# Kernel tuning notes

Hardware: AMD Instinct MI355X
Metric: run time of the kernel (lower is better)

The kernel has to match this reference:

```python
import jax, jax.numpy as jnp
import numpy as np

B, T, S, H, V, L = 32, 64, 128, 512, 32000, 2  # batch, tgt_len, src_len, d_model, vocab, n_layers


def setup_inputs() -> dict:
    key = jax.random.key(0)
    ks = jax.random.split(key, 14)
    sc = 1.0 / np.sqrt(H)
    tgt = jax.random.randint(ks[0], (B, T), 0, V, dtype=jnp.int32)
    h0 = jax.random.normal(ks[1], (L, B, H), jnp.float32)
    c0 = jax.random.normal(ks[2], (L, B, H), jnp.float32)
    encoder_outputs = jax.random.normal(ks[3], (B, S, H), jnp.float32)
    emb = (jax.random.normal(ks[4], (V, H), jnp.float32) * 0.02).at[0].set(0.0)  # pad_idx=0 row zeroed
    W_ih = jax.random.normal(ks[5], (L, 4 * H, H), jnp.float32) * sc  # gate order i,f,g,o (torch)
    W_hh = jax.random.normal(ks[6], (L, 4 * H, H), jnp.float32) * sc
    b_ih = jax.random.normal(ks[7], (L, 4 * H), jnp.float32) * sc
    b_hh = jax.random.normal(ks[8], (L, 4 * H), jnp.float32) * sc
    Wc = jax.random.normal(ks[9], (H, 2 * H), jnp.float32) * sc
    bc = jax.random.normal(ks[10], (H,), jnp.float32) * sc
    Wo = jax.random.normal(ks[11], (V, H), jnp.float32) * sc
    bo = jax.random.normal(ks[12], (V,), jnp.float32) * sc
    return dict(tgt=tgt, h0=h0, c0=c0, encoder_outputs=encoder_outputs, emb=emb,
                W_ih=W_ih, W_hh=W_hh, b_ih=b_ih, b_hh=b_hh, Wc=Wc, bc=bc, Wo=Wo, bo=bo)


def reference(tgt, h0, c0, encoder_outputs, emb, W_ih, W_hh, b_ih, b_hh, Wc, bc, Wo, bo):
    n_layers = W_ih.shape[0]

    def step(carry, token):
        h, c = carry  # each [L, B, H]
        x = emb[token]  # [B, H]
        hs, cs = [], []
        for l in range(n_layers):  # small fixed structural loop
            gates = x @ W_ih[l].T + b_ih[l] + h[l] @ W_hh[l].T + b_hh[l]  # [B, 4H]
            i_g, f_g, g_g, o_g = jnp.split(gates, 4, axis=-1)
            c_new = jax.nn.sigmoid(f_g) * c[l] + jax.nn.sigmoid(i_g) * jnp.tanh(g_g)
            h_new = jax.nn.sigmoid(o_g) * jnp.tanh(c_new)
            hs.append(h_new)
            cs.append(c_new)
            x = h_new
        out = x  # [B, H] top-layer output
        # Luong (dot) attention over encoder outputs
        scores = jnp.einsum('bh,bsh->bs', out, encoder_outputs)
        attn = jax.nn.softmax(scores, axis=-1)
        context = jnp.einsum('bs,bsh->bh', attn, encoder_outputs)
        out_att = jnp.tanh(jnp.concatenate([out, context], axis=-1) @ Wc.T + bc)
        pred = out_att @ Wo.T + bo  # [B, V]
        return (jnp.stack(hs), jnp.stack(cs)), pred

    (h, c), preds = jax.lax.scan(step, (h0, c0), tgt.T)  # scan over time (T-major)
    return preds.transpose(1, 0, 2), h, c  # [B, T, V], hidden state
```

## Files before the change

### kernel.cpp

```cpp
#include <hip/hip_runtime.h>
#include <hip/hip_bf16.h>

#define Bz 32
#define Tz 64
#define Sz 128
#define Hz 512
#define Vz 32000
#define G4 2048
#define NBLK 256
#define NPH 65

#define A_RLX __ATOMIC_RELAXED
#define SC_AG __HIP_MEMORY_SCOPE_AGENT

using bf16x8 = __attribute__((ext_vector_type(8))) short;
using f32x4  = __attribute__((ext_vector_type(4))) float;

__device__ __forceinline__ unsigned short f2bf(float f){
  unsigned int u = __float_as_uint(f);
  u += 0x7fffu + ((u >> 16) & 1u);
  return (unsigned short)(u >> 16);
}
__device__ __forceinline__ float sigf(float x){ return 1.f/(1.f + expf(-x)); }

__device__ __forceinline__ void stc(float* p, float v){
  __hip_atomic_store(p, v, A_RLX, SC_AG);
}
__device__ __forceinline__ float ldc(const float* p){
  return __hip_atomic_load(p, A_RLX, SC_AG);
}

__device__ __forceinline__ void g_arrive(unsigned* bar, int bid, unsigned e){
  asm volatile("s_waitcnt vmcnt(0)" ::: "memory");
  __syncthreads();
  if (threadIdx.x == 0)
    __hip_atomic_store(&bar[bid], e, A_RLX, SC_AG);
}
__device__ __forceinline__ void g_wait(unsigned* bar, unsigned e){
  if (threadIdx.x < 64){
    const int lane = threadIdx.x;
    for (;;){
      int ok = 1;
      #pragma unroll
      for (int i = 0; i < 4; i++){
        unsigned v = __hip_atomic_load(&bar[lane + i*64], A_RLX, SC_AG);
        ok &= ((int)(v - e) >= 0);
      }
      if (__all(ok)) break;
      __builtin_amdgcn_s_sleep(1);
    }
  }
  __syncthreads();
  __builtin_amdgcn_sched_barrier(0);
}

__device__ __forceinline__ void xreduce(float (&a)[32], int lane){
  #pragma unroll
  for (int j = 0; j < 32; j++) a[j] += __shfl_xor(a[j], 32);
  #pragma unroll
  for (int st = 0; st < 5; st++){
    const int o = 16 >> st;
    bool hi = (lane & o) != 0;
    float tmp[16];
    #pragma unroll
    for (int j = 0; j < o; j++){
      float lo_v = a[j], hi_v = a[j + o];
      float sent = hi ? lo_v : hi_v;
      float recv = __shfl_xor(sent, o);
      tmp[j] = (hi ? hi_v : lo_v) + recv;
    }
    #pragma unroll
    for (int j = 0; j < o; j++) a[j] = tmp[j];
  }
}

__device__ __forceinline__ void stage2c(float* dA, const float* sA,
                                        float* dB, const float* sB, int tid){
  float ra[32], rb[32];
  #pragma unroll
  for (int i = 0; i < 32; i++) ra[i] = ldc(sA + tid + i*512);
  #pragma unroll
  for (int i = 0; i < 32; i++) rb[i] = ldc(sB + tid + i*512);
  #pragma unroll
  for (int i = 0; i < 32; i++){
    int f = tid + i*512;
    dA[(f >> 9)*520 + (f & 511)] = ra[i];
  }
  #pragma unroll
  for (int i = 0; i < 32; i++){
    int f = tid + i*512;
    dB[(f >> 9)*520 + (f & 511)] = rb[i];
  }
}

__global__ __launch_bounds__(256) void init_state_v8(const float* __restrict__ h0,
    float* __restrict__ h0p, float* __restrict__ h1p, unsigned int* __restrict__ bar){
  int i = blockIdx.x*256 + threadIdx.x;
  if (i < 16384) h0p[16384 + i] = h0[i];
  else           h1p[3*16384 + (i - 16384)] = h0[i];
  if (i < 512) bar[i] = 0u;
}

__global__ __launch_bounds__(256) void conv_bf16_kernel(const float* __restrict__ src,
    unsigned short* __restrict__ dst){
  int i = (blockIdx.x*256 + threadIdx.x)*4;
  float4 v = *(const float4*)(src + i);
  ushort4 o;
  o.x = f2bf(v.x); o.y = f2bf(v.y); o.z = f2bf(v.z); o.w = f2bf(v.w);
  *(ushort4*)(dst + i) = o;
}

__global__ __launch_bounds__(256) void pack_l0_v3(const float* __restrict__ W,
    float* __restrict__ out){
  int idx4 = blockIdx.x*256 + threadIdx.x;
  int r = idx4 >> 7, k4 = idx4 & 127;
  int srow = (r & 3)*Hz + (r >> 2);
  ((float4*)out)[idx4] = ((const float4*)W)[srow*128 + k4];
}
__global__ __launch_bounds__(256) void pack_l1_v3(const float* __restrict__ Wi,
    const float* __restrict__ Wh, float* __restrict__ out){
  int idx4 = blockIdx.x*256 + threadIdx.x;
  int r = idx4 >> 8, k4 = idx4 & 255;
  int srow = (r & 3)*Hz + (r >> 2);
  float4 v = (k4 < 128) ? ((const float4*)Wi)[srow*128 + k4]
                        : ((const float4*)Wh)[srow*128 + (k4 - 128)];
  ((float4*)out)[idx4] = v;
}

__global__ __launch_bounds__(256) void x0g_v3(const int* __restrict__ tgt,
    const float* __restrict__ emb, const float* __restrict__ W,
    const float* __restrict__ bi, const float* __restrict__ bh,
    float* __restrict__ out){
  __shared__ float As[32][68], Bs[32][68];
  __shared__ int tok_s[64];
  int tid = threadIdx.x;
  int m0 = blockIdx.y*64, n0 = blockIdx.x*64;
  if (tid < 64){ int tb = m0 + tid; tok_s[tid] = tgt[(tb & 31)*Tz + (tb >> 5)]; }
  __syncthreads();
  int lm = tid >> 2, lk = (tid & 3)*8;
  int ty = tid >> 4, tx = tid & 15;
  float acc[4][4] = {{0.f}};
  for (int kt = 0; kt < 16; kt++){
    float4 a0 = *(const float4*)(emb + (size_t)tok_s[lm]*Hz + kt*32 + lk);
    float4 a1 = *(const float4*)(emb + (size_t)tok_s[lm]*Hz + kt*32 + lk + 4);
    float4 b0 = *(const float4*)(W   + (size_t)(n0+lm)*Hz + kt*32 + lk);
    float4 b1 = *(const float4*)(W   + (size_t)(n0+lm)*Hz + kt*32 + lk + 4);
    __syncthreads();
    As[lk+0][lm]=a0.x; As[lk+1][lm]=a0.y; As[lk+2][lm]=a0.z; As[lk+3][lm]=a0.w;
    As[lk+4][lm]=a1.x; As[lk+5][lm]=a1.y; As[lk+6][lm]=a1.z; As[lk+7][lm]=a1.w;
    Bs[lk+0][lm]=b0.x; Bs[lk+1][lm]=b0.y; Bs[lk+2][lm]=b0.z; Bs[lk+3][lm]=b0.w;
    Bs[lk+4][lm]=b1.x; Bs[lk+5][lm]=b1.y; Bs[lk+6][lm]=b1.z; Bs[lk+7][lm]=b1.w;
    __syncthreads();
    #pragma unroll
    for (int k = 0; k < 32; k++){
      float4 av = *(const float4*)&As[k][ty*4];
      float4 bv = *(const float4*)&Bs[k][tx*4];
      acc[0][0]+=av.x*bv.x; acc[0][1]+=av.x*bv.y; acc[0][2]+=av.x*bv.z; acc[0][3]+=av.x*bv.w;
      acc[1][0]+=av.y*bv.x; acc[1][1]+=av.y*bv.y; acc[1][2]+=av.y*bv.z; acc[1][3]+=av.y*bv.w;
      acc[2][0]+=av.z*bv.x; acc[2][1]+=av.z*bv.y; acc[2][2]+=av.z*bv.z; acc[2][3]+=av.z*bv.w;
      acc[3][0]+=av.w*bv.x; acc[3][1]+=av.w*bv.y; acc[3][2]+=av.w*bv.z; acc[3][3]+=av.w*bv.w;
    }
  }
  #pragma unroll
  for (int j = 0; j < 4; j++){
    int col = n0 + tx*4 + j;
    float bias = bi[col] + bh[col];
    #pragma unroll
    for (int i = 0; i < 4; i++){
      int tb = m0 + ty*4 + i;
      int tt = tb >> 5, bb = tb & 31;
      out[((size_t)tt*2048 + col)*32 + bb] = acc[i][j] + bias;
    }
  }
}

__global__ __launch_bounds__(512, 1) void decoder_persist_v9(
    const float* __restrict__ Wp0, const float* __restrict__ Wp1,
    const float* x0gT,
    const float* __restrict__ bi1, const float* __restrict__ bh1,
    const float* __restrict__ c0in,
    float* __restrict__ h0p,
    float* __restrict__ h1p,
    float* hist,
    float* __restrict__ cbuf,
    unsigned* __restrict__ bar){
  extern __shared__ float sm[];
  float* hstA = sm;
  float* hstB = sm + 16640;
  float* gsA  = sm + 33280;
  float* gsB  = sm + 33792;
  float4* hA4 = (float4*)hstA;
  float4* hB4 = (float4*)hstB;

  const int bid = blockIdx.x, tid = threadIdx.x;
  const int w4 = tid >> 6, lane = tid & 63;
  const int kh = w4 >> 2, rpair = w4 & 3;
  const int r0 = bid*8 + rpair*2, r1 = r0 + 1;

  const float4* Wp0_4 = (const float4*)Wp0;
  const float4* Wp1_4 = (const float4*)Wp1;
  float4 w0A  = Wp0_4[r0*128 + kh*64 + lane];
  float4 w0B  = Wp0_4[r1*128 + kh*64 + lane];
  float4 w1xA = Wp1_4[r0*256 +       kh*64 + lane];
  float4 w1xB = Wp1_4[r1*256 +       kh*64 + lane];
  float4 w1hA = Wp1_4[r0*256 + 128 + kh*64 + lane];
  float4 w1hB = Wp1_4[r1*256 + 128 + kh*64 + lane];
  float bs_i=0.f, bs_f=0.f, bs_g=0.f, bs_o=0.f;
  float c0_reg=0.f, c1_reg=0.f;
  float xgi=0.f, xgf=0.f, xgg=0.f, xgo=0.f;
  if (tid < 64){
    int b = tid & 31, u = bid*2 + (tid >> 5);
    bs_i = bi1[u]        + bh1[u];
    bs_f = bi1[512+u]    + bh1[512+u];
    bs_g = bi1[1024+u]   + bh1[1024+u];
    bs_o = bi1[1536+u]   + bh1[1536+u];
    c0_reg = c0in[b*512 + u];
    c1_reg = c0in[16384 + b*512 + u];
    xgi = x0gT[(u       )*32 + b];
    xgf = x0gT[(512  + u)*32 + b];
    xgg = x0gT[(1024 + u)*32 + b];
    xgo = x0gT[(1536 + u)*32 + b];
  }
  __syncthreads();

  for (int tau = 0; tau < NPH; ++tau){
    stage2c(hstA, h0p + ((tau+1)&1)*16384, hstB, h1p + ((tau+2)&3)*16384, tid);
    __syncthreads();
    {
      float aL0A[32], aL0B[32], aL1A[32], aL1B[32];
      #pragma unroll
      for (int b = 0; b < 32; b++){ aL0A[b]=0.f; aL0B[b]=0.f; aL1A[b]=0.f; aL1B[b]=0.f; }
      const float4* pA = hA4 + kh*64 + lane;
      const float4* pB = hB4 + kh*64 + lane;
      #pragma unroll
      for (int b = 0; b < 32; b++){
        float4 ha = pA[b*130];
        float4 hb = pB[b*130];
        aL0A[b] = fmaf(ha.x,w0A.x, fmaf(ha.y,w0A.y, fmaf(ha.z,w0A.z, fmaf(ha.w,w0A.w, aL0A[b]))));
        aL0B[b] = fmaf(ha.x,w0B.x, fmaf(ha.y,w0B.y, fmaf(ha.z,w0B.z, fmaf(ha.w,w0B.w, aL0B[b]))));
        float t1 = fmaf(ha.x,w1xA.x, fmaf(ha.y,w1xA.y, fmaf(ha.z,w1xA.z, fmaf(ha.w,w1xA.w, aL1A[b]))));
        aL1A[b] = fmaf(hb.x,w1hA.x, fmaf(hb.y,w1hA.y, fmaf(hb.z,w1hA.z, fmaf(hb.w,w1hA.w, t1))));
        float t2 = fmaf(ha.x,w1xB.x, fmaf(ha.y,w1xB.y, fmaf(ha.z,w1xB.z, fmaf(ha.w,w1xB.w, aL1B[b]))));
        aL1B[b] = fmaf(hb.x,w1hB.x, fmaf(hb.y,w1hB.y, fmaf(hb.z,w1hB.z, fmaf(hb.w,w1hB.w, t2))));
      }
      xreduce(aL0A, lane); xreduce(aL0B, lane);
      gsA[kh*256 + (rpair*2 + (lane >= 32 ? 1 : 0))*32 + (lane & 31)] = (lane < 32) ? aL0A[0] : aL0B[0];
      xreduce(aL1A, lane); xreduce(aL1B, lane);
      gsB[kh*256 + (rpair*2 + (lane >= 32 ? 1 : 0))*32 + (lane & 31)] = (lane < 32) ? aL1A[0] : aL1B[0];
    }
    __syncthreads();
    float hv1 = 0.f;
    if (tid < 64){
      int ul = tid >> 5, b = tid & 31, u = bid*2 + ul, rl = ul*4;
      if (tau < 64){
        float gi = gsA[(rl+0)*32+b] + gsA[256+(rl+0)*32+b] + xgi;
        float gf = gsA[(rl+1)*32+b] + gsA[256+(rl+1)*32+b] + xgf;
        float gg = gsA[(rl+2)*32+b] + gsA[256+(rl+2)*32+b] + xgg;
        float go = gsA[(rl+3)*32+b] + gsA[256+(rl+3)*32+b] + xgo;
        float cn = sigf(gf)*c0_reg + sigf(gi)*tanhf(gg);
        c0_reg = cn;
        stc(h0p + (tau&1)*16384 + b*512 + u, sigf(go)*tanhf(cn));
      }
      if (tau >= 1){
        float gi = gsB[(rl+0)*32+b] + gsB[256+(rl+0)*32+b] + bs_i;
        float gf = gsB[(rl+1)*32+b] + gsB[256+(rl+1)*32+b] + bs_f;
        float gg = gsB[(rl+2)*32+b] + gsB[256+(rl+2)*32+b] + bs_g;
        float go = gsB[(rl+3)*32+b] + gsB[256+(rl+3)*32+b] + bs_o;
        float cn = sigf(gf)*c1_reg + sigf(gi)*tanhf(gg);
        c1_reg = cn;
        hv1 = sigf(go)*tanhf(cn);
        stc(h1p + ((tau-1)&3)*16384 + b*512 + u, hv1);
      }
    }
    g_arrive(bar, bid, (unsigned)(tau + 1));
    if (tid < 64){
      int b = tid & 31, u = bid*2 + (tid >> 5);
      if (tau >= 1)
        hist[(size_t)(tau-1)*65536 + b*512 + u] = hv1;
      if (tau + 1 < 64){
        const float* xg = x0gT + (size_t)(tau+1)*65536;
        xgi = xg[(u       )*32 + b];
        xgf = xg[(512  + u)*32 + b];
        xgg = xg[(1024 + u)*32 + b];
        xgo = xg[(1536 + u)*32 + b];
      }
    }
    g_wait(bar, (unsigned)(tau + 1));
  }
  if (tid < 64){
    int b = tid & 31, u = bid*2 + (tid >> 5);
    cbuf[b*512 + u] = c0_reg;
    cbuf[16384 + b*512 + u] = c1_reg;
  }
}

__global__ __launch_bounds__(256) void attn_batch(const float* hist,
    const float* __restrict__ enc, float* ctxout){
  __shared__ float h_s[Hz], e_s[Sz], red_s[2];
  const int bid = blockIdx.x;
  const int t = bid >> 5, b = bid & 31, tid = threadIdx.x;
  const float* h1 = hist + (size_t)t*65536 + b*512;
  *(float2*)(h_s + tid*2) = *(const float2*)(h1 + tid*2);
  __syncthreads();
  {
    int s = tid >> 1, half = tid & 1;
    const float4* e4 = (const float4*)(enc + ((size_t)b*Sz + s)*Hz + half*256);
    const float4* h4 = (const float4*)(h_s + half*256);
    float a = 0.f;
    #pragma unroll 16
    for (int k = 0; k < 64; k++){
      float4 e = e4[k], h = h4[k];
      a += e.x*h.x + e.y*h.y + e.z*h.z + e.w*h.w;
    }
    a += __shfl_xor(a, 1);
    if (!half) e_s[s] = a;
  }
  __syncthreads();
  if (tid < 64){
    float v = fmaxf(e_s[tid], e_s[tid+64]);
    #pragma unroll
    for (int o = 32; o; o >>= 1) v = fmaxf(v, __shfl_xor(v, o));
    if (tid == 0) red_s[0] = v;
  }
  __syncthreads();
  if (tid < Sz) e_s[tid] = expf(e_s[tid] - red_s[0]);
  __syncthreads();
  if (tid < 64){
    float v = e_s[tid] + e_s[tid+64];
    #pragma unroll
    for (int o = 32; o; o >>= 1) v += __shfl_xor(v, o);
    if (tid == 0) red_s[1] = v;
  }
  __syncthreads();
  {
    float inv = 1.f/red_s[1];
    int k0 = tid*2;
    float c0 = 0.f, c1 = 0.f;
    const float* ep = enc + (size_t)b*Sz*Hz + k0;
    #pragma unroll 8
    for (int s = 0; s < Sz; s++){
      float2 ev = *(const float2*)(ep + (size_t)s*Hz);
      float pr = e_s[s];
      c0 += pr*ev.x; c1 += pr*ev.y;
    }
    float2 o; o.x = c0*inv; o.y = c1*inv;
    *(float2*)(ctxout + (size_t)t*65536 + 32768 + b*512 + k0) = o;
  }
}

__global__ __launch_bounds__(256) void outatt_gemm(const float* xg,
    const float* __restrict__ Wc, const float* __restrict__ bc,
    unsigned short* __restrict__ oa){
  __shared__ float As[32][68], Bs[32][68];
  int tid = threadIdx.x;
  int m0 = blockIdx.y*64, n0 = blockIdx.x*64;
  int lm = tid >> 2, lk = (tid & 3)*8;
  int ty = tid >> 4, tx = tid & 15;
  int am = m0 + lm, at = am >> 5, ab = am & 31;
  const float* arow = xg + (size_t)at*65536 + ab*512;
  float acc[4][4] = {{0.f}};
  for (int kt = 0; kt < 32; kt++){
    int k = kt*32 + lk;
    const float* asrc = (k < 512) ? (arow + k) : (arow + 32768 + (k - 512));
    float4 a0 = *(const float4*)asrc;
    float4 a1 = *(const float4*)(asrc + 4);
    float4 b0 = *(const float4*)(Wc + (size_t)(n0+lm)*1024 + k);
    float4 b1 = *(const float4*)(Wc + (size_t)(n0+lm)*1024 + k + 4);
    __syncthreads();
    As[lk+0][lm]=a0.x; As[lk+1][lm]=a0.y; As[lk+2][lm]=a0.z; As[lk+3][lm]=a0.w;
    As[lk+4][lm]=a1.x; As[lk+5][lm]=a1.y; As[lk+6][lm]=a1.z; As[lk+7][lm]=a1.w;
    Bs[lk+0][lm]=b0.x; Bs[lk+1][lm]=b0.y; Bs[lk+2][lm]=b0.z; Bs[lk+3][lm]=b0.w;
    Bs[lk+4][lm]=b1.x; Bs[lk+5][lm]=b1.y; Bs[lk+6][lm]=b1.z; Bs[lk+7][lm]=b1.w;
    __syncthreads();
    #pragma unroll
    for (int k2 = 0; k2 < 32; k2++){
      float4 av = *(const float4*)&As[k2][ty*4];
      float4 bv = *(const float4*)&Bs[k2][tx*4];
      acc[0][0]+=av.x*bv.x; acc[0][1]+=av.x*bv.y; acc[0][2]+=av.x*bv.z; acc[0][3]+=av.x*bv.w;
      acc[1][0]+=av.y*bv.x; acc[1][1]+=av.y*bv.y; acc[1][2]+=av.y*bv.z; acc[1][3]+=av.y*bv.w;
      acc[2][0]+=av.z*bv.x; acc[2][1]+=av.z*bv.y; acc[2][2]+=av.z*bv.z; acc[2][3]+=av.z*bv.w;
      acc[3][0]+=av.w*bv.x; acc[3][1]+=av.w*bv.y; acc[3][2]+=av.w*bv.z; acc[3][3]+=av.w*bv.w;
    }
  }
  #pragma unroll
  for (int j = 0; j < 4; j++){
    int col = n0 + tx*4 + j;
    float bias = bc[col];
    #pragma unroll
    for (int i = 0; i < 4; i++){
      int m = m0 + ty*4 + i;
      int t = m >> 5, b = m & 31;
      oa[((size_t)(b*64 + t))*512 + col] = f2bf(tanhf(acc[i][j] + bias));
    }
  }
}

__global__ __launch_bounds__(256) void pred_gemm_v3(const unsigned short* __restrict__ A,
    const unsigned short* __restrict__ Bm, const float* __restrict__ bo,
    float* __restrict__ out){
  __shared__ unsigned short As[128*32];
  __shared__ unsigned short Bs[128*32];
  int bid = blockIdx.x;
  int xcd = bid & 7, lin = bid >> 3;
  int ntile = xcd*32 + (lin >> 4);
  int mtile = lin & 15;
  if (ntile >= 250) return;
  int n0 = ntile*128, m0 = mtile*128;
  int tid = threadIdx.x, lane = tid & 63, wid = tid >> 6;
  f32x4 acc[4][4];
  #pragma unroll
  for (int i = 0; i < 4; i++)
    #pragma unroll
    for (int j = 0; j < 4; j++)
      #pragma unroll
      for (int r = 0; r < 4; r++) acc[i][j][r] = 0.f;

  int wm = wid >> 1, wn = wid & 1;
  int r16 = lane & 15, kgr = lane >> 4;

  for (int kt = 0; kt < Hz/32; kt++){
    __syncthreads();
    #pragma unroll
    for (int call = 0; call < 2; call++){
      int c = call*256 + tid;
      int row = c >> 2, kg = c & 3;
      int kgs = kg ^ ((row >> 1) & 3);
      *(int4*)&As[row*32 + kgs*8] = *(const int4*)(A  + (size_t)(m0+row)*Hz + kt*32 + kg*8);
      *(int4*)&Bs[row*32 + kgs*8] = *(const int4*)(Bm + (size_t)(n0+row)*Hz + kt*32 + kg*8);
    }
    __syncthreads();
    bf16x8 aF[4], bF[4];
    #pragma unroll
    for (int i = 0; i < 4; i++){
      int ra = wm*64 + i*16 + r16;
      int rb = wn*64 + i*16 + r16;
      aF[i] = *(const bf16x8*)&As[ra*32 + (kgr ^ ((ra>>1)&3))*8];
      bF[i] = *(const bf16x8*)&Bs[rb*32 + (kgr ^ ((rb>>1)&3))*8];
    }
    #pragma unroll
    for (int i = 0; i < 4; i++)
      #pragma unroll
      for (int j = 0; j < 4; j++)
        acc[i][j] = __builtin_amdgcn_mfma_f32_16x16x32_bf16(aF[i], bF[j], acc[i][j], 0, 0, 0);
  }

  int rg = lane >> 4;
  #pragma unroll
  for (int i = 0; i < 4; i++)
    #pragma unroll
    for (int j = 0; j < 4; j++){
      int col = n0 + wn*64 + j*16 + r16;
      float bias = bo[col];
      #pragma unroll
      for (int r = 0; r < 4; r++){
        int row = m0 + wm*64 + i*16 + rg*4 + r;
        out[(size_t)row*Vz + col] = acc[i][j][r] + bias;
      }
    }
}

__global__ __launch_bounds__(256) void copy_hc_v4(const float* __restrict__ h0fin,
    const float* __restrict__ h1fin, const float* __restrict__ cbuf,
    float* __restrict__ out_hc){
  int i = blockIdx.x*256 + threadIdx.x;
  float v;
  if (i < 16384)      v = h0fin[i];
  else if (i < 32768) v = h1fin[i-16384];
  else                v = cbuf[i-32768];
  out_hc[i] = v;
}

extern "C" void kernel_launch(void* const* d_in, const int* in_sizes, int n_in,
                              void* d_out, int out_size, void* d_ws, size_t ws_size,
                              hipStream_t stream){
  const int*   tgt = (const int*)  d_in[0];
  const float* h0  = (const float*)d_in[1];
  const float* c0  = (const float*)d_in[2];
  const float* enc = (const float*)d_in[3];
  const float* emb = (const float*)d_in[4];
  const float* Wih = (const float*)d_in[5];
  const float* Whh = (const float*)d_in[6];
  const float* bih = (const float*)d_in[7];
  const float* bhh = (const float*)d_in[8];
  const float* Wc  = (const float*)d_in[9];
  const float* bc  = (const float*)d_in[10];
  const float* Wo  = (const float*)d_in[11];
  const float* bo  = (const float*)d_in[12];
  float* out = (float*)d_out;

  float* x0g  = (float*)d_ws;
  float* h0p  = x0g  + 4194304;
  float* h1p  = h0p  + 32768;
  float* cbuf = h1p  + 65536;
  float* Wp0  = cbuf + 32768;
  float* Wp1  = Wp0  + 1048576;
  unsigned int* bar = (unsigned int*)(Wp1 + 2097152);
  unsigned short* oa    = (unsigned short*)(bar + 512);
  unsigned short* wo_bf = oa + 1048576;

  const int DLDS_BYTES = 34304 * 4;
  hipFuncSetAttribute((const void*)decoder_persist_v9,
      hipFuncAttributeMaxDynamicSharedMemorySize, DLDS_BYTES);

  init_state_v8<<<128, 256, 0, stream>>>(h0, h0p, h1p, bar);
  conv_bf16_kernel<<<16000, 256, 0, stream>>>(Wo, wo_bf);
  pack_l0_v3<<<1024, 256, 0, stream>>>(Whh, Wp0);
  pack_l1_v3<<<2048, 256, 0, stream>>>(Wih + (size_t)G4*Hz, Whh + (size_t)G4*Hz, Wp1);
  x0g_v3<<<dim3(32, 32), 256, 0, stream>>>(tgt, emb, Wih, bih, bhh, x0g);

  decoder_persist_v9<<<NBLK, 512, DLDS_BYTES, stream>>>(
      Wp0, Wp1, x0g, bih + G4, bhh + G4, c0,
      h0p, h1p, x0g, cbuf, (unsigned int*)bar);

  attn_batch<<<2048, 256, 0, stream>>>(x0g, enc, x0g);
  outatt_gemm<<<dim3(8, 32), 256, 0, stream>>>(x0g, Wc, bc, oa);
  pred_gemm_v3<<<4096, 256, 0, stream>>>(oa, wo_bf, bo, out);
  copy_hc_v4<<<256, 256, 0, stream>>>(h0p + 16384, x0g + (size_t)63*65536, cbuf,
                                      out + (size_t)Bz*Tz*Vz);

  (void)in_sizes; (void)n_in; (void)out_size; (void)ws_size;
}
```

Baseline: 1.285 ms.

## Split persistent decoder grid barrier into separate per-layer arrival arrays

Replaces the single global barrier per phase with two flag arrays, one for layer 0 and one for layer 1. Each layer stage now waits only on the flags it depends on before staging its hidden state. Layer 0 of the next step can then proceed while other blocks are still finishing layer 1. This adds an extra barrier round and shared-memory staging per phase, and lengthens the spin sleep, which may add wake-up latency.

```diff
diff --git a/kernel.cpp b/kernel.cpp
--- a/kernel.cpp
+++ b/kernel.cpp
@@ -30,24 +30,24 @@
   return __hip_atomic_load(p, A_RLX, SC_AG);
 }
 
-__device__ __forceinline__ void g_arrive(unsigned* bar, int bid, unsigned e){
+__device__ __forceinline__ void g_arrive(unsigned* arr, int bid, unsigned e){
   asm volatile("s_waitcnt vmcnt(0)" ::: "memory");
   __syncthreads();
   if (threadIdx.x == 0)
-    __hip_atomic_store(&bar[bid], e, A_RLX, SC_AG);
-}
-__device__ __forceinline__ void g_wait(unsigned* bar, unsigned e){
+    __hip_atomic_store(&arr[bid], e, A_RLX, SC_AG);
+}
+__device__ __forceinline__ void g_check(const unsigned* arr, unsigned e){
   if (threadIdx.x < 64){
     const int lane = threadIdx.x;
     for (;;){
       int ok = 1;
       #pragma unroll
       for (int i = 0; i < 4; i++){
-        unsigned v = __hip_atomic_load(&bar[lane + i*64], A_RLX, SC_AG);
+        unsigned v = __hip_atomic_load(&arr[lane + i*64], A_RLX, SC_AG);
         ok &= ((int)(v - e) >= 0);
       }
       if (__all(ok)) break;
-      __builtin_amdgcn_s_sleep(1);
+      __builtin_amdgcn_s_sleep(4);
     }
   }
   __syncthreads();
@@ -74,26 +74,18 @@
   }
 }
 
-__device__ __forceinline__ void stage2c(float* dA, const float* sA,
-                                        float* dB, const float* sB, int tid){
-  float ra[32], rb[32];
-  #pragma unroll
-  for (int i = 0; i < 32; i++) ra[i] = ldc(sA + tid + i*512);
-  #pragma unroll
-  for (int i = 0; i < 32; i++) rb[i] = ldc(sB + tid + i*512);
+__device__ __forceinline__ void stage1c(float* dst, const float* src, int tid){
+  float r[32];
+  #pragma unroll
+  for (int i = 0; i < 32; i++) r[i] = ldc(src + tid + i*512);
   #pragma unroll
   for (int i = 0; i < 32; i++){
     int f = tid + i*512;
-    dA[(f >> 9)*520 + (f & 511)] = ra[i];
-  }
-  #pragma unroll
-  for (int i = 0; i < 32; i++){
-    int f = tid + i*512;
-    dB[(f >> 9)*520 + (f & 511)] = rb[i];
-  }
-}
-
-__global__ __launch_bounds__(256) void init_state_v8(const float* __restrict__ h0,
+    dst[(f >> 9)*520 + (f & 511)] = r[i];
+  }
+}
+
+__global__ __launch_bounds__(256) void init_state_v11(const float* __restrict__ h0,
     float* __restrict__ h0p, float* __restrict__ h1p, unsigned int* __restrict__ bar){
   int i = blockIdx.x*256 + threadIdx.x;
   if (i < 16384) h0p[16384 + i] = h0[i];
@@ -174,7 +166,7 @@
   }
 }
 
-__global__ __launch_bounds__(512, 1) void decoder_persist_v9(
+__global__ __launch_bounds__(512, 1) void decoder_persist_v11(
     const float* __restrict__ Wp0, const float* __restrict__ Wp1,
     const float* x0gT,
     const float* __restrict__ bi1, const float* __restrict__ bh1,
@@ -191,6 +183,8 @@
   float* gsB  = sm + 33792;
   float4* hA4 = (float4*)hstA;
   float4* hB4 = (float4*)hstB;
+  unsigned* arrA = bar;
+  unsigned* arrB = bar + 256;
 
   const int bid = blockIdx.x, tid = threadIdx.x;
   const int w4 = tid >> 6, lane = tid & 63;
@@ -224,55 +218,70 @@
   __syncthreads();
 
   for (int tau = 0; tau < NPH; ++tau){
-    stage2c(hstA, h0p + ((tau+1)&1)*16384, hstB, h1p + ((tau+2)&3)*16384, tid);
-    __syncthreads();
-    {
-      float aL0A[32], aL0B[32], aL1A[32], aL1B[32];
-      #pragma unroll
-      for (int b = 0; b < 32; b++){ aL0A[b]=0.f; aL0B[b]=0.f; aL1A[b]=0.f; aL1B[b]=0.f; }
+    if (tau >= 1) g_check(arrA, (unsigned)tau);
+    stage1c(hstA, h0p + ((tau+1)&1)*16384, tid);
+    __syncthreads();
+    if (tau < 64){
+      float a0[32], a1[32];
+      #pragma unroll
+      for (int b = 0; b < 32; b++){ a0[b]=0.f; a1[b]=0.f; }
+      const float4* pA = hA4 + kh*64 + lane;
+      #pragma unroll
+      for (int b = 0; b < 32; b++){
+        float4 ha = pA[b*130];
+        a0[b] = fmaf(ha.x,w0A.x, fmaf(ha.y,w0A.y, fmaf(ha.z,w0A.z, fmaf(ha.w,w0A.w, a0[b]))));
+        a1[b] = fmaf(ha.x,w0B.x, fmaf(ha.y,w0B.y, fmaf(ha.z,w0B.z, fmaf(ha.w,w0B.w, a1[b]))));
+      }
+      xreduce(a0, lane); xreduce(a1, lane);
+      gsA[kh*256 + (rpair*2 + (lane >= 32 ? 1 : 0))*32 + (lane & 31)] = (lane < 32) ? a0[0] : a1[0];
+    }
+    __syncthreads();
+    if (tid < 64 && tau < 64){
+      int ul = tid >> 5, b = tid & 31, u = bid*2 + ul, rl = ul*4;
+      float gi = gsA[(rl+0)*32+b] + gsA[256+(rl+0)*32+b] + xgi;
+      float gf = gsA[(rl+1)*32+b] + gsA[256+(rl+1)*32+b] + xgf;
+      float gg = gsA[(rl+2)*32+b] + gsA[256+(rl+2)*32+b] + xgg;
+      float go = gsA[(rl+3)*32+b] + gsA[256+(rl+3)*32+b] + xgo;
+      float cn = sigf(gf)*c0_reg + sigf(gi)*tanhf(gg);
+      c0_reg = cn;
+      stc(h0p + (tau&1)*16384 + b*512 + u, sigf(go)*tanhf(cn));
+    }
+    g_arrive(arrA, bid, (unsigned)(tau + 1));
+    if (tau >= 2) g_check(arrB, (unsigned)(tau - 1));
+    stage1c(hstB, h1p + ((tau+2)&3)*16384, tid);
+    __syncthreads();
+    if (tau >= 1){
+      float a0[32], a1[32];
+      #pragma unroll
+      for (int b = 0; b < 32; b++){ a0[b]=0.f; a1[b]=0.f; }
       const float4* pA = hA4 + kh*64 + lane;
       const float4* pB = hB4 + kh*64 + lane;
       #pragma unroll
       for (int b = 0; b < 32; b++){
         float4 ha = pA[b*130];
         float4 hb = pB[b*130];
-        aL0A[b] = fmaf(ha.x,w0A.x, fmaf(ha.y,w0A.y, fmaf(ha.z,w0A.z, fmaf(ha.w,w0A.w, aL0A[b]))));
-        aL0B[b] = fmaf(ha.x,w0B.x, fmaf(ha.y,w0B.y, fmaf(ha.z,w0B.z, fmaf(ha.w,w0B.w, aL0B[b]))));
-        float t1 = fmaf(ha.x,w1xA.x, fmaf(ha.y,w1xA.y, fmaf(ha.z,w1xA.z, fmaf(ha.w,w1xA.w, aL1A[b]))));
-        aL1A[b] = fmaf(hb.x,w1hA.x, fmaf(hb.y,w1hA.y, fmaf(hb.z,w1hA.z, fmaf(hb.w,w1hA.w, t1))));
-        float t2 = fmaf(ha.x,w1xB.x, fmaf(ha.y,w1xB.y, fmaf(ha.z,w1xB.z, fmaf(ha.w,w1xB.w, aL1B[b]))));
-        aL1B[b] = fmaf(hb.x,w1hB.x, fmaf(hb.y,w1hB.y, fmaf(hb.z,w1hB.z, fmaf(hb.w,w1hB.w, t2))));
+        float t1 = fmaf(ha.x,w1xA.x, fmaf(ha.y,w1xA.y, fmaf(ha.z,w1xA.z, fmaf(ha.w,w1xA.w, a0[b]))));
+        a0[b] = fmaf(hb.x,w1hA.x, fmaf(hb.y,w1hA.y, fmaf(hb.z,w1hA.z, fmaf(hb.w,w1hA.w, t1))));
+        float t2 = fmaf(ha.x,w1xB.x, fmaf(ha.y,w1xB.y, fmaf(ha.z,w1xB.z, fmaf(ha.w,w1xB.w, a1[b]))));
+        a1[b] = fmaf(hb.x,w1hB.x, fmaf(hb.y,w1hB.y, fmaf(hb.z,w1hB.z, fmaf(hb.w,w1hB.w, t2))));
       }
-      xreduce(aL0A, lane); xreduce(aL0B, lane);
-      gsA[kh*256 + (rpair*2 + (lane >= 32 ? 1 : 0))*32 + (lane & 31)] = (lane < 32) ? aL0A[0] : aL0B[0];
-      xreduce(aL1A, lane); xreduce(aL1B, lane);
-      gsB[kh*256 + (rpair*2 + (lane >= 32 ? 1 : 0))*32 + (lane & 31)] = (lane < 32) ? aL1A[0] : aL1B[0];
+      xreduce(a0, lane); xreduce(a1, lane);
+      gsB[kh*256 + (rpair*2 + (lane >= 32 ? 1 : 0))*32 + (lane & 31)] = (lane < 32) ? a0[0] : a1[0];
     }
     __syncthreads();
     float hv1 = 0.f;
-    if (tid < 64){
+    if (tid < 64 && tau >= 1){
       int ul = tid >> 5, b = tid & 31, u = bid*2 + ul, rl = ul*4;
-      if (tau < 64){
-        float gi = gsA[(rl+0)*32+b] + gsA[256+(rl+0)*32+b] + xgi;
-        float gf = gsA[(rl+1)*32+b] + gsA[256+(rl+1)*32+b] + xgf;
-        float gg = gsA[(rl+2)*32+b] + gsA[256+(rl+2)*32+b] + xgg;
-        float go = gsA[(rl+3)*32+b] + gsA[256+(rl+3)*32+b] + xgo;
-        float cn = sigf(gf)*c0_reg + sigf(gi)*tanhf(gg);
-        c0_reg = cn;
-        stc(h0p + (tau&1)*16384 + b*512 + u, sigf(go)*tanhf(cn));
-      }
-      if (tau >= 1){
-        float gi = gsB[(rl+0)*32+b] + gsB[256+(rl+0)*32+b] + bs_i;
-        float gf = gsB[(rl+1)*32+b] + gsB[256+(rl+1)*32+b] + bs_f;
-        float gg = gsB[(rl+2)*32+b] + gsB[256+(rl+2)*32+b] + bs_g;
-        float go = gsB[(rl+3)*32+b] + gsB[256+(rl+3)*32+b] + bs_o;
-        float cn = sigf(gf)*c1_reg + sigf(gi)*tanhf(gg);
-        c1_reg = cn;
-        hv1 = sigf(go)*tanhf(cn);
-        stc(h1p + ((tau-1)&3)*16384 + b*512 + u, hv1);
-      }
-    }
-    g_arrive(bar, bid, (unsigned)(tau + 1));
+      float gi = gsB[(rl+0)*32+b] + gsB[256+(rl+0)*32+b] + bs_i;
+      float gf = gsB[(rl+1)*32+b] + gsB[256+(rl+1)*32+b] + bs_f;
+      float gg = gsB[(rl+2)*32+b] + gsB[256+(rl+2)*32+b] + bs_g;
+      float go = gsB[(rl+3)*32+b] + gsB[256+(rl+3)*32+b] + bs_o;
+      float cn = sigf(gf)*c1_reg + sigf(gi)*tanhf(gg);
+      c1_reg = cn;
+      hv1 = sigf(go)*tanhf(cn);
+      stc(h1p + ((tau-1)&3)*16384 + b*512 + u, hv1);
+    }
+    g_arrive(arrB, bid, (unsigned)tau);
     if (tid < 64){
       int b = tid & 31, u = bid*2 + (tid >> 5);
       if (tau >= 1)
@@ -285,7 +294,6 @@
         xgo = xg[(1536 + u)*32 + b];
       }
     }
-    g_wait(bar, (unsigned)(tau + 1));
   }
   if (tid < 64){
     int b = tid & 31, u = bid*2 + (tid >> 5);
@@ -499,16 +507,16 @@
   unsigned short* wo_bf = oa + 1048576;
 
   const int DLDS_BYTES = 34304 * 4;
-  hipFuncSetAttribute((const void*)decoder_persist_v9,
+  hipFuncSetAttribute((const void*)decoder_persist_v11,
       hipFuncAttributeMaxDynamicSharedMemorySize, DLDS_BYTES);
 
-  init_state_v8<<<128, 256, 0, stream>>>(h0, h0p, h1p, bar);
+  init_state_v11<<<128, 256, 0, stream>>>(h0, h0p, h1p, bar);
   conv_bf16_kernel<<<16000, 256, 0, stream>>>(Wo, wo_bf);
   pack_l0_v3<<<1024, 256, 0, stream>>>(Whh, Wp0);
   pack_l1_v3<<<2048, 256, 0, stream>>>(Wih + (size_t)G4*Hz, Whh + (size_t)G4*Hz, Wp1);
   x0g_v3<<<dim3(32, 32), 256, 0, stream>>>(tgt, emb, Wih, bih, bhh, x0g);
 
-  decoder_persist_v9<<<NBLK, 512, DLDS_BYTES, stream>>>(
+  decoder_persist_v11<<<NBLK, 512, DLDS_BYTES, stream>>>(
       Wp0, Wp1, x0g, bih + G4, bhh + G4, c0,
       h0p, h1p, x0g, cbuf, (unsigned int*)bar);
 
```

Measured after the change: 1.129 ms. -12.2%, faster.
